# Performance work log

Hardware: AMD Instinct MI355X
Metric: run time of the kernel (lower is better)

The kernel has to match this reference:

```python
import jax, jax.numpy as jnp
import numpy as np

B, S, D = 2, 2048, 1024
N, M, HD = 16, 4, 64          # query heads, kv heads, head dim
G = N // M                    # GQA group size
V = 32000
GIN = 12                      # gate input dim
ROPE_THETA = 1024.0
ROT = int(HD * 0.5)           # partial rotary dim = 32
EPS = 1e-6
STD = 0.006


def setup_inputs() -> dict:
    key = jax.random.key(0)
    ks = jax.random.split(key, 10)
    tn = lambda k, shape: (STD * jax.random.truncated_normal(k, -3, 3, shape)).astype(jnp.float32)
    return {
        "x": jax.random.normal(ks[0], (B, S, D), jnp.float32),
        "token_ids": jax.random.randint(ks[1], (B, S), 0, V),
        "mask": jnp.tril(jnp.ones((S, S), dtype=bool)),  # causal
        "w_q": tn(ks[2], (D, N * HD)),
        "w_k": tn(ks[3], (D, M * HD)),
        "w_v": tn(ks[4], (D, M * HD)),
        "w_o": tn(ks[5], (N * HD, D)),  # zeros at init; random for a meaningful baseline
        "ve_embed": tn(ks[6], (V, M * HD)),
        "value_lambda": jnp.full((), 0.5, jnp.float32),
        "ve_lambda": jnp.full((), 0.5, jnp.float32),
        "ve_gate": tn(ks[7], (GIN, M)),
        "attn_gate": tn(ks[8], (GIN, N)),
    }


def _qk_norm(t):
    var = jnp.mean(jnp.square(t.astype(jnp.float32)), axis=-1, keepdims=True)
    return (t * jax.lax.rsqrt(var + EPS)).astype(t.dtype)


def _rope(t):
    # partial rotary: rotate first ROT dims only
    half = ROT // 2
    inv_freq = 1.0 / ROPE_THETA ** (jnp.arange(half, dtype=jnp.float32) / half)
    ang = jnp.arange(S, dtype=jnp.float32)[:, None] * inv_freq[None, :]
    cos = jnp.cos(ang)[None, :, None, :]  # [1,S,1,half]
    sin = jnp.sin(ang)[None, :, None, :]
    rot, pas = t[..., :ROT], t[..., ROT:]
    x1, x2 = jnp.split(rot, 2, axis=-1)
    return jnp.concatenate([x1 * cos - x2 * sin, x2 * cos + x1 * sin, pas], axis=-1)


def reference(x, token_ids, mask, w_q, w_k, w_v, w_o, ve_embed,
              value_lambda, ve_lambda, ve_gate, attn_gate):
    q = (x @ w_q).reshape(B, S, N, HD)
    k = (x @ w_k).reshape(B, S, M, HD)
    v = (x @ w_v).reshape(B, S, M, HD)
    q = _rope(_qk_norm(q))
    k = _rope(_qk_norm(k))

    # value-embedding lambda mixing with sigmoid gate
    ve = ve_embed[token_ids].reshape(B, S, M, HD)
    ve_g = 2.0 * jax.nn.sigmoid(x[..., :GIN] @ ve_gate)       # [B,S,M]
    v = value_lambda * v + ve_lambda * ve_g[..., None] * ve

    # GQA causal attention (group q heads over kv heads, no kv repeat)
    qg = q.reshape(B, S, M, G, HD)
    scale = 1.0 / np.sqrt(HD).astype(np.float32)
    scores = jnp.einsum('bqmgd,bkmd->bmgqk', qg, k) * scale   # [B,M,G,S,S]
    scores = jnp.where(mask[None, None, None], scores, jnp.float32(-1e30))
    p = jax.nn.softmax(scores, axis=-1)
    attn = jnp.einsum('bmgqk,bkmd->bqmgd', p, v).reshape(B, S, N, HD)

    # output sigmoid gate then out-projection
    a_g = 2.0 * jax.nn.sigmoid(x[..., :GIN] @ attn_gate)      # [B,S,N]
    attn = a_g[..., None] * attn
    return attn.reshape(B, S, N * HD) @ w_o
```

## Files before the change

### kernel.cpp

```cpp
#include <hip/hip_runtime.h>
#include <math.h>

#define S_LEN 2048
#define NHEADS 16
#define KVH 4

typedef __attribute__((ext_vector_type(8))) _Float16 half8;
typedef __attribute__((ext_vector_type(4))) _Float16 half4;
typedef __attribute__((ext_vector_type(2))) __fp16 fp16x2;
typedef __attribute__((ext_vector_type(4))) float f32x4;

__device__ inline void gld16(const void* g, void* l) {
  __builtin_amdgcn_global_load_lds(
      (const __attribute__((address_space(1))) unsigned int*)g,
      (__attribute__((address_space(3))) unsigned int*)l, 16, 0, 0);
}

__global__ __launch_bounds__(256) void setup_fused(
    const float* __restrict__ wq, const float* __restrict__ wk,
    const float* __restrict__ wv, const float* __restrict__ wo,
    const float* __restrict__ x, const float* __restrict__ attn_gate,
    _Float16* __restrict__ wqkvT, _Float16* __restrict__ woT,
    float2* __restrict__ costab, float* __restrict__ ag,
    _Float16* __restrict__ xh)
{
  const int t = threadIdx.x;
  int L = blockIdx.x;

  if (L >= 1024) {
    const size_t i = ((size_t)(L - 1024) * 256 + t) * 16;
    #pragma unroll
    for (int c = 0; c < 2; c++) {
      float4 f0 = *(const float4*)(x + i + c * 8);
      float4 f1 = *(const float4*)(x + i + c * 8 + 4);
      half8 h;
      h[0] = (_Float16)f0.x; h[1] = (_Float16)f0.y; h[2] = (_Float16)f0.z; h[3] = (_Float16)f0.w;
      h[4] = (_Float16)f1.x; h[5] = (_Float16)f1.y; h[6] = (_Float16)f1.z; h[7] = (_Float16)f1.w;
      *(half8*)(xh + i + c * 8) = h;
    }
    return;
  }
  if (L >= 768) {
    const int row = (L - 768) * 16 + (t >> 4);
    const int n = t & 15;
    float z = 0.f;
    #pragma unroll
    for (int i = 0; i < 12; ++i) z += x[(size_t)row * 1024 + i] * attn_gate[i * NHEADS + n];
    ag[(size_t)row * NHEADS + n] = 2.f / (1.f + __expf(-z));
    return;
  }
  if (L >= 640) {
    const int gi = (L - 640) * 256 + t;
    const int s = gi >> 4, i = gi & 15;
    const float ang = (float)s * exp2f(-0.625f * (float)i);
    float c, sn;
    sincosf(ang, &sn, &c);
    costab[gi] = make_float2(c, sn);
    return;
  }

  const float* in; _Float16* out; int C, ct, rt;
  if (L < 256)      { in = wq; out = wqkvT;                       C = 1024; ct = (L & 15) * 64; rt = (L >> 4) * 64; }
  else if (L < 320) { L -= 256; in = wk; out = wqkvT + (size_t)1024 * 1024; C = 256; ct = (L & 3) * 64; rt = (L >> 2) * 64; }
  else if (L < 384) { L -= 320; in = wv; out = wqkvT + (size_t)1280 * 1024; C = 256; ct = (L & 3) * 64; rt = (L >> 2) * 64; }
  else              { L -= 384; in = wo; out = woT;               C = 1024; ct = (L & 15) * 64; rt = (L >> 4) * 64; }

  __shared__ float Ls[64][65];
  {
    const int r = t >> 2, cs = (t & 3) << 4;
    const float* src = in + (size_t)(rt + r) * C + ct + cs;
    #pragma unroll
    for (int j = 0; j < 16; j += 4) {
      float4 v = *(const float4*)(src + j);
      Ls[r][cs + j] = v.x; Ls[r][cs + j + 1] = v.y;
      Ls[r][cs + j + 2] = v.z; Ls[r][cs + j + 3] = v.w;
    }
  }
  __syncthreads();
  {
    const int c = t >> 2, rs = (t & 3) << 4;
    half8 h0, h1;
    #pragma unroll
    for (int j = 0; j < 8; j++) h0[j] = (_Float16)Ls[rs + j][c];
    #pragma unroll
    for (int j = 0; j < 8; j++) h1[j] = (_Float16)Ls[rs + 8 + j][c];
    _Float16* dst = out + (size_t)(ct + c) * 1024 + rt + rs;
    *(half8*)dst = h0;
    *(half8*)(dst + 8) = h1;
  }
}

template<typename OUT_T, bool EPI>
__global__ __launch_bounds__(256) void gemm_k(
    const _Float16* __restrict__ A, const _Float16* __restrict__ BT,
    OUT_T* __restrict__ C, int M, int N, int K, int lda,
    const float2* __restrict__ costab)
{
  __shared__ _Float16 lds[16384];
  const int t = threadIdx.x;
  const int w = t >> 6, l = t & 63;
  const int lg = l >> 4, ll = l & 15;
  const int bm = blockIdx.y * 128, bn = blockIdx.x * 128;
  const int wr = (w >> 1) * 64, wc = (w & 1) * 64;
  const int srow = t >> 2, sslot = t & 3;

  f32x4 acc[4][4] = {};

  auto stage = [&](int k0, int buf) {
    char* Ab = (char*)lds + buf * 8192;
    char* Bb = (char*)lds + 16384 + buf * 8192;
    const int so = (sslot ^ (srow & 3)) << 3;
    gld16(A  + (size_t)(bm + srow)      * lda + k0 + so, Ab + w * 1024);
    gld16(A  + (size_t)(bm + srow + 64) * lda + k0 + so, Ab + 4096 + w * 1024);
    gld16(BT + (size_t)(bn + srow)      * K   + k0 + so, Bb + w * 1024);
    gld16(BT + (size_t)(bn + srow + 64) * K   + k0 + so, Bb + 4096 + w * 1024);
  };

  stage(0, 0);
  __syncthreads();

  int buf = 0;
  for (int k0 = 0; k0 < K; k0 += 32) {
    if (k0 + 32 < K) stage(k0 + 32, buf ^ 1);

    const char* Ab = (const char*)lds + buf * 8192;
    const char* Bb = (const char*)lds + 16384 + buf * 8192;
    half8 af[4], bfr[4];
    #pragma unroll
    for (int mt = 0; mt < 4; mt++) {
      const int row = wr + mt * 16 + ll;
      af[mt] = *(const half8*)(Ab + row * 64 + ((lg ^ (row & 3)) << 4));
    }
    #pragma unroll
    for (int nt = 0; nt < 4; nt++) {
      const int row = wc + nt * 16 + ll;
      bfr[nt] = *(const half8*)(Bb + row * 64 + ((lg ^ (row & 3)) << 4));
    }
    __builtin_amdgcn_s_setprio(1);
    #pragma unroll
    for (int mt = 0; mt < 4; mt++)
      #pragma unroll
      for (int nt = 0; nt < 4; nt++)
        acc[mt][nt] = __builtin_amdgcn_mfma_f32_16x16x32_f16(af[mt], bfr[nt], acc[mt][nt], 0, 0, 0);
    __builtin_amdgcn_s_setprio(0);

    __syncthreads();
    buf ^= 1;
  }

  if constexpr (EPI) {
    const int col0 = bn + wc;
    const int head = col0 >> 6;
    const bool isv = head >= 20;
    const float qs = (head < 16) ? 0.18033688f : 1.0f;
    #pragma unroll
    for (int mt = 0; mt < 4; mt++) {
      if (isv) {
        #pragma unroll
        for (int r = 0; r < 4; r++) {
          const size_t row = (size_t)bm + wr + mt * 16 + lg * 4 + r;
          #pragma unroll
          for (int nt = 0; nt < 4; nt++)
            C[row * N + col0 + nt * 16 + ll] = (OUT_T)acc[mt][nt][r];
        }
      } else {
        float ss[4];
        #pragma unroll
        for (int r = 0; r < 4; r++)
          ss[r] = acc[mt][0][r] * acc[mt][0][r] + acc[mt][1][r] * acc[mt][1][r]
                + acc[mt][2][r] * acc[mt][2][r] + acc[mt][3][r] * acc[mt][3][r];
        #pragma unroll
        for (int mi = 0; mi < 4; mi++) {
          const int msk = 1 << mi;
          #pragma unroll
          for (int r = 0; r < 4; r++) ss[r] += __shfl_xor(ss[r], msk);
        }
        #pragma unroll
        for (int r = 0; r < 4; r++) {
          const size_t row = (size_t)bm + wr + mt * 16 + lg * 4 + r;
          const float inv = rsqrtf(ss[r] * (1.0f / 64.0f) + 1e-6f) * qs;
          const float2 cs2 = costab[(row & (S_LEN - 1)) * 16 + ll];
          const float a0 = acc[mt][0][r] * inv, a1 = acc[mt][1][r] * inv;
          C[row * N + col0 +      ll] = (OUT_T)(a0 * cs2.x - a1 * cs2.y);
          C[row * N + col0 + 16 + ll] = (OUT_T)(a1 * cs2.x + a0 * cs2.y);
          C[row * N + col0 + 32 + ll] = (OUT_T)(acc[mt][2][r] * inv);
          C[row * N + col0 + 48 + ll] = (OUT_T)(acc[mt][3][r] * inv);
        }
      }
    }
  } else {
    #pragma unroll
    for (int mt = 0; mt < 4; mt++) {
      #pragma unroll
      for (int r = 0; r < 4; r++) {
        const size_t row = (size_t)bm + wr + mt * 16 + lg * 4 + r;
        #pragma unroll
        for (int nt = 0; nt < 4; nt++) {
          const int col = bn + wc + nt * 16 + ll;
          if constexpr (sizeof(OUT_T) == 2) C[row * N + col] = (OUT_T)(_Float16)acc[mt][nt][r];
          else                              C[row * N + col] = acc[mt][nt][r];
        }
      }
    }
  }
}

__global__ __launch_bounds__(256) void vtrans_mix(
    const _Float16* __restrict__ qkv, const float* __restrict__ x,
    const int* __restrict__ token_ids, const float* __restrict__ ve_embed,
    const float* __restrict__ ve_gate, const float* __restrict__ vlam,
    const float* __restrict__ velam, _Float16* __restrict__ vT)
{
  __shared__ _Float16 Ls[64][72];
  __shared__ float veg[64];
  __shared__ int toks[64];
  const int st = blockIdx.x * 64;
  const int bm = blockIdx.y;
  const int b = bm >> 2, m = bm & 3;
  const int t = threadIdx.x;

  if (t < 64) {
    const size_t row_g = (size_t)b * S_LEN + st + t;
    toks[t] = token_ids[row_g];
    float z = 0.f;
    #pragma unroll
    for (int i = 0; i < 12; ++i) z += x[row_g * 1024 + i] * ve_gate[i * KVH + m];
    veg[t] = velam[0] * 2.f / (1.f + __expf(-z));
  }
  __syncthreads();
  {
    const int sr = t >> 2, ds = (t & 3) << 4;
    const float vl = vlam[0];
    const _Float16* src = qkv + ((size_t)(b * S_LEN + st + sr)) * 1536 + 1280 + m * 64 + ds;
    const float* ves = ve_embed + (size_t)toks[sr] * 256 + m * 64 + ds;
    half8 v0 = *(const half8*)src;
    half8 v1 = *(const half8*)(src + 8);
    const float g = veg[sr];
    #pragma unroll
    for (int q4 = 0; q4 < 4; q4++) {
      float4 ev = *(const float4*)(ves + q4 * 4);
      const int o0 = q4 * 4;
      Ls[sr][ds + o0 + 0] = (_Float16)(vl * (float)((o0 + 0 < 8) ? v0[o0 + 0] : v1[o0 - 8]) + g * ev.x);
      Ls[sr][ds + o0 + 1] = (_Float16)(vl * (float)((o0 + 1 < 8) ? v0[o0 + 1] : v1[o0 - 7]) + g * ev.y);
      Ls[sr][ds + o0 + 2] = (_Float16)(vl * (float)((o0 + 2 < 8) ? v0[o0 + 2] : v1[o0 - 6]) + g * ev.z);
      Ls[sr][ds + o0 + 3] = (_Float16)(vl * (float)((o0 + 3 < 8) ? v0[o0 + 3] : v1[o0 - 5]) + g * ev.w);
    }
  }
  __syncthreads();
  {
    const int dr = t >> 2, ssl = (t & 3) << 4;
    half8 o0, o1;
    #pragma unroll
    for (int j = 0; j < 8; j++) { o0[j] = Ls[ssl + j][dr]; o1[j] = Ls[ssl + 8 + j][dr]; }
    _Float16* dst = vT + ((size_t)bm * 64 + dr) * S_LEN + st + ssl;
    *(half8*)dst = o0;
    *(half8*)(dst + 8) = o1;
  }
}

__global__ __launch_bounds__(256) void attn_mfma(
    _Float16* __restrict__ qkv, const _Float16* __restrict__ vT,
    const float* __restrict__ ag)
{
  const int L = blockIdx.x;
  const int qt = 31 - (L >> 5);
  const int b = (L >> 4) & 1;
  const int n = L & 15;
  const int m = n >> 2;

  const int t = threadIdx.x, w = t >> 6, l = t & 63;
  const int lg = l >> 4, ll = l & 15;

  __shared__ _Float16 lds[20480];

  const int qbase = qt * 64 + w * 16;
  const size_t qrow_g = (size_t)(b * S_LEN) + qbase;

  half8 qa[2];
  #pragma unroll
  for (int s = 0; s < 2; s++)
    qa[s] = *(const half8*)(qkv + (qrow_g + ll) * 1536 + n * 64 + s * 32 + lg * 8);

  float agr[4];
  #pragma unroll
  for (int r = 0; r < 4; r++)
    agr[r] = ag[(qrow_g + lg * 4 + r) * NHEADS + n];

  half8 ones;
  #pragma unroll
  for (int i = 0; i < 8; i++) ones[i] = (_Float16)1.0f;

  f32x4 o[4] = {};
  f32x4 ol = {};

  const int srow = l >> 3, sslot = l & 7;
  const int q_loc = w * 16 + ll;

  auto stage = [&](int kt, int buf) {
    #pragma unroll
    for (int i = 0; i < 2; i++) {
      const int kr = w * 16 + i * 8 + srow;
      const size_t kg = ((size_t)(b * S_LEN + kt * 64 + kr)) * 1536 + 1024 + m * 64
                        + ((sslot ^ (kr & 7)) << 3);
      gld16(qkv + kg, (char*)lds + buf * 8192 + w * 2048 + i * 1024);
      const int vr = w * 16 + i * 8 + srow;
      const size_t vg = ((size_t)((b * KVH + m) * 64 + vr)) * S_LEN + kt * 64
                        + ((sslot ^ (vr & 7)) << 3);
      gld16(vT + vg, (char*)lds + 16384 + buf * 8192 + w * 2048 + i * 1024);
    }
  };

  stage(0, 0);
  __syncthreads();

  for (int kt = 0; kt <= qt; kt++) {
    const int cur = kt & 1;
    if (kt < qt) stage(kt + 1, cur ^ 1);

    const char* Ksb = (const char*)lds + cur * 8192;
    const char* Vsb = (const char*)lds + 16384 + cur * 8192;
    char* Psb = (char*)lds + 32768;

    f32x4 sc[4];
    #pragma unroll
    for (int kf = 0; kf < 4; kf++) {
      sc[kf][0] = -11.6f; sc[kf][1] = -11.6f; sc[kf][2] = -11.6f; sc[kf][3] = -11.6f;
    }
    __builtin_amdgcn_s_setprio(1);
    #pragma unroll
    for (int s = 0; s < 2; s++)
      #pragma unroll
      for (int kf = 0; kf < 4; kf++) {
        const int krow = kf * 16 + ll;
        const half8 kb = *(const half8*)(Ksb + krow * 128
                          + (((4 * s + lg) ^ (krow & 7)) << 4));
        sc[kf] = __builtin_amdgcn_mfma_f32_16x16x32_f16(kb, qa[s], sc[kf], 0, 0, 0);
      }
    __builtin_amdgcn_s_setprio(0);

    if (kt == qt) {
      const int qg = qbase + ll;
      #pragma unroll
      for (int kf = 0; kf < 4; kf++)
        #pragma unroll
        for (int r = 0; r < 4; r++)
          if (kt * 64 + kf * 16 + 4 * lg + r > qg) sc[kf][r] = -1e30f;
    }

    #pragma unroll
    for (int kf = 0; kf < 4; kf++) {
      union { fp16x2 h2[2]; half4 h4; } P;
      P.h2[0] = __builtin_amdgcn_cvt_pkrtz(exp2f(sc[kf][0]), exp2f(sc[kf][1]));
      P.h2[1] = __builtin_amdgcn_cvt_pkrtz(exp2f(sc[kf][2]), exp2f(sc[kf][3]));
      const int slot = (2 * kf + (lg >> 1)) ^ (q_loc & 7);
      *(half4*)(Psb + q_loc * 128 + slot * 16 + (lg & 1) * 8) = P.h4;
    }

    __builtin_amdgcn_s_setprio(1);
    #pragma unroll
    for (int s = 0; s < 2; s++) {
      const half8 pa = *(const half8*)(Psb + q_loc * 128
                        + (((4 * s + lg) ^ (q_loc & 7)) << 4));
      ol = __builtin_amdgcn_mfma_f32_16x16x32_f16(pa, ones, ol, 0, 0, 0);
      #pragma unroll
      for (int df = 0; df < 4; df++) {
        const int vrow = df * 16 + ll;
        const half8 vb = *(const half8*)(Vsb + vrow * 128
                          + (((4 * s + lg) ^ (vrow & 7)) << 4));
        o[df] = __builtin_amdgcn_mfma_f32_16x16x32_f16(pa, vb, o[df], 0, 0, 0);
      }
    }
    __builtin_amdgcn_s_setprio(0);

    __syncthreads();
  }

  #pragma unroll
  for (int r = 0; r < 4; r++) {
    const size_t qrow = qrow_g + lg * 4 + r;
    const float scale = agr[r] / ol[r];
    #pragma unroll
    for (int df = 0; df < 4; df++)
      qkv[qrow * 1536 + n * 64 + df * 16 + ll] = (_Float16)(o[df][r] * scale);
  }
}

extern "C" void kernel_launch(void* const* d_in, const int* in_sizes, int n_in,
                              void* d_out, int out_size, void* d_ws, size_t ws_size,
                              hipStream_t stream) {
  const float* x         = (const float*)d_in[0];
  const int*   token_ids = (const int*)d_in[1];
  const float* w_q       = (const float*)d_in[3];
  const float* w_k       = (const float*)d_in[4];
  const float* w_v       = (const float*)d_in[5];
  const float* w_o       = (const float*)d_in[6];
  const float* ve_embed  = (const float*)d_in[7];
  const float* vlam      = (const float*)d_in[8];
  const float* velam     = (const float*)d_in[9];
  const float* ve_gate   = (const float*)d_in[10];
  const float* attn_gate = (const float*)d_in[11];
  float* out = (float*)d_out;

  char* p = (char*)d_ws;
  _Float16* wqkvT = (_Float16*)p; p += (size_t)1536 * 1024 * 2;
  _Float16* woT   = (_Float16*)p; p += (size_t)1024 * 1024 * 2;
  _Float16* qkv   = (_Float16*)p; p += (size_t)4096 * 1536 * 2;
  _Float16* vTb   = (_Float16*)p; p += (size_t)8 * 64 * S_LEN * 2;
  float*    ag    = (float*)p;    p += (size_t)4096 * NHEADS * 4;

  _Float16* xh = (_Float16*)d_out;
  float2* costab = (float2*)((char*)d_out + (size_t)12 * 1024 * 1024);

  dim3 blk(256);
  setup_fused<<<dim3(2048), blk, 0, stream>>>(w_q, w_k, w_v, w_o, x, attn_gate,
                                              wqkvT, woT, costab, ag, xh);

  gemm_k<_Float16, true><<<dim3(12, 32), blk, 0, stream>>>(
      xh, wqkvT, qkv, 4096, 1536, 1024, 1024, costab);

  vtrans_mix<<<dim3(32, 8), blk, 0, stream>>>(qkv, x, token_ids, ve_embed,
                                              ve_gate, vlam, velam, vTb);

  attn_mfma<<<dim3(1024), blk, 0, stream>>>(qkv, vTb, ag);

  gemm_k<float, false><<<dim3(8, 32), blk, 0, stream>>>(
      qkv, woT, out, 4096, 1024, 1024, 1536, nullptr);
}
```

Before: 100.0 us.

## Give each attention wave two query tiles and halve block size to 128

The attention kernel now runs 2 waves per block instead of 4, and each wave handles 32 query rows as two 16-row fragments. Each K and V fragment read from LDS is reused by two MFMAs, and staging issues four loads per thread instead of two. The aim is to cut LDS read traffic per MFMA and increase instruction-level parallelism. In exchange each wave holds more registers and there are fewer waves per block to hide latency.

```diff
diff --git a/kernel.cpp b/kernel.cpp
--- a/kernel.cpp
+++ b/kernel.cpp
@@ -258,7 +258,7 @@
   }
 }
 
-__global__ __launch_bounds__(256) void attn_mfma(
+__global__ __launch_bounds__(128) void attn_mfma(
     _Float16* __restrict__ qkv, const _Float16* __restrict__ vT,
     const float* __restrict__ ag)
 {
@@ -273,40 +273,42 @@
 
   __shared__ _Float16 lds[20480];
 
-  const int qbase = qt * 64 + w * 16;
+  const int qbase = qt * 64 + w * 32;
   const size_t qrow_g = (size_t)(b * S_LEN) + qbase;
 
-  half8 qa[2];
+  half8 qa[2][2];
   #pragma unroll
-  for (int s = 0; s < 2; s++)
-    qa[s] = *(const half8*)(qkv + (qrow_g + ll) * 1536 + n * 64 + s * 32 + lg * 8);
-
-  float agr[4];
+  for (int qf = 0; qf < 2; qf++)
+    #pragma unroll
+    for (int s = 0; s < 2; s++)
+      qa[qf][s] = *(const half8*)(qkv + (qrow_g + qf * 16 + ll) * 1536 + n * 64 + s * 32 + lg * 8);
+
+  float agr[2][4];
   #pragma unroll
-  for (int r = 0; r < 4; r++)
-    agr[r] = ag[(qrow_g + lg * 4 + r) * NHEADS + n];
+  for (int qf = 0; qf < 2; qf++)
+    #pragma unroll
+    for (int r = 0; r < 4; r++)
+      agr[qf][r] = ag[(qrow_g + qf * 16 + lg * 4 + r) * NHEADS + n];
 
   half8 ones;
   #pragma unroll
   for (int i = 0; i < 8; i++) ones[i] = (_Float16)1.0f;
 
-  f32x4 o[4] = {};
-  f32x4 ol = {};
+  f32x4 o[2][4] = {};
+  f32x4 ol[2] = {};
 
   const int srow = l >> 3, sslot = l & 7;
-  const int q_loc = w * 16 + ll;
 
   auto stage = [&](int kt, int buf) {
     #pragma unroll
-    for (int i = 0; i < 2; i++) {
-      const int kr = w * 16 + i * 8 + srow;
+    for (int i = 0; i < 4; i++) {
+      const int kr = w * 32 + i * 8 + srow;
       const size_t kg = ((size_t)(b * S_LEN + kt * 64 + kr)) * 1536 + 1024 + m * 64
                         + ((sslot ^ (kr & 7)) << 3);
-      gld16(qkv + kg, (char*)lds + buf * 8192 + w * 2048 + i * 1024);
-      const int vr = w * 16 + i * 8 + srow;
-      const size_t vg = ((size_t)((b * KVH + m) * 64 + vr)) * S_LEN + kt * 64
-                        + ((sslot ^ (vr & 7)) << 3);
-      gld16(vT + vg, (char*)lds + 16384 + buf * 8192 + w * 2048 + i * 1024);
+      gld16(qkv + kg, (char*)lds + buf * 8192 + w * 4096 + i * 1024);
+      const size_t vg = ((size_t)((b * KVH + m) * 64 + kr)) * S_LEN + kt * 64
+                        + ((sslot ^ (kr & 7)) << 3);
+      gld16(vT + vg, (char*)lds + 16384 + buf * 8192 + w * 4096 + i * 1024);
     }
   };
 
@@ -321,11 +323,14 @@
     const char* Vsb = (const char*)lds + 16384 + cur * 8192;
     char* Psb = (char*)lds + 32768;
 
-    f32x4 sc[4];
-    #pragma unroll
-    for (int kf = 0; kf < 4; kf++) {
-      sc[kf][0] = -11.6f; sc[kf][1] = -11.6f; sc[kf][2] = -11.6f; sc[kf][3] = -11.6f;
-    }
+    f32x4 sc[2][4];
+    #pragma unroll
+    for (int qf = 0; qf < 2; qf++)
+      #pragma unroll
+      for (int kf = 0; kf < 4; kf++) {
+        sc[qf][kf][0] = -11.6f; sc[qf][kf][1] = -11.6f;
+        sc[qf][kf][2] = -11.6f; sc[qf][kf][3] = -11.6f;
+      }
     __builtin_amdgcn_s_setprio(1);
     #pragma unroll
     for (int s = 0; s < 2; s++)
@@ -334,40 +339,54 @@
         const int krow = kf * 16 + ll;
         const half8 kb = *(const half8*)(Ksb + krow * 128
                           + (((4 * s + lg) ^ (krow & 7)) << 4));
-        sc[kf] = __builtin_amdgcn_mfma_f32_16x16x32_f16(kb, qa[s], sc[kf], 0, 0, 0);
+        sc[0][kf] = __builtin_amdgcn_mfma_f32_16x16x32_f16(kb, qa[0][s], sc[0][kf], 0, 0, 0);
+        sc[1][kf] = __builtin_amdgcn_mfma_f32_16x16x32_f16(kb, qa[1][s], sc[1][kf], 0, 0, 0);
       }
     __builtin_amdgcn_s_setprio(0);
 
     if (kt == qt) {
-      const int qg = qbase + ll;
-      #pragma unroll
-      for (int kf = 0; kf < 4; kf++)
-        #pragma unroll
-        for (int r = 0; r < 4; r++)
-          if (kt * 64 + kf * 16 + 4 * lg + r > qg) sc[kf][r] = -1e30f;
-    }
-
-    #pragma unroll
-    for (int kf = 0; kf < 4; kf++) {
-      union { fp16x2 h2[2]; half4 h4; } P;
-      P.h2[0] = __builtin_amdgcn_cvt_pkrtz(exp2f(sc[kf][0]), exp2f(sc[kf][1]));
-      P.h2[1] = __builtin_amdgcn_cvt_pkrtz(exp2f(sc[kf][2]), exp2f(sc[kf][3]));
-      const int slot = (2 * kf + (lg >> 1)) ^ (q_loc & 7);
-      *(half4*)(Psb + q_loc * 128 + slot * 16 + (lg & 1) * 8) = P.h4;
+      #pragma unroll
+      for (int qf = 0; qf < 2; qf++) {
+        const int qg = qbase + qf * 16 + ll;
+        #pragma unroll
+        for (int kf = 0; kf < 4; kf++)
+          #pragma unroll
+          for (int r = 0; r < 4; r++)
+            if (kt * 64 + kf * 16 + 4 * lg + r > qg) sc[qf][kf][r] = -1e30f;
+      }
+    }
+
+    #pragma unroll
+    for (int qf = 0; qf < 2; qf++) {
+      const int q_loc = w * 32 + qf * 16 + ll;
+      #pragma unroll
+      for (int kf = 0; kf < 4; kf++) {
+        union { fp16x2 h2[2]; half4 h4; } P;
+        P.h2[0] = __builtin_amdgcn_cvt_pkrtz(exp2f(sc[qf][kf][0]), exp2f(sc[qf][kf][1]));
+        P.h2[1] = __builtin_amdgcn_cvt_pkrtz(exp2f(sc[qf][kf][2]), exp2f(sc[qf][kf][3]));
+        const int slot = (2 * kf + (lg >> 1)) ^ (q_loc & 7);
+        *(half4*)(Psb + q_loc * 128 + slot * 16 + (lg & 1) * 8) = P.h4;
+      }
     }
 
     __builtin_amdgcn_s_setprio(1);
     #pragma unroll
     for (int s = 0; s < 2; s++) {
-      const half8 pa = *(const half8*)(Psb + q_loc * 128
-                        + (((4 * s + lg) ^ (q_loc & 7)) << 4));
-      ol = __builtin_amdgcn_mfma_f32_16x16x32_f16(pa, ones, ol, 0, 0, 0);
+      half8 pa[2];
+      #pragma unroll
+      for (int qf = 0; qf < 2; qf++) {
+        const int prow = w * 32 + qf * 16 + ll;
+        pa[qf] = *(const half8*)(Psb + prow * 128 + (((4 * s + lg) ^ (prow & 7)) << 4));
+      }
+      ol[0] = __builtin_amdgcn_mfma_f32_16x16x32_f16(pa[0], ones, ol[0], 0, 0, 0);
+      ol[1] = __builtin_amdgcn_mfma_f32_16x16x32_f16(pa[1], ones, ol[1], 0, 0, 0);
       #pragma unroll
       for (int df = 0; df < 4; df++) {
         const int vrow = df * 16 + ll;
         const half8 vb = *(const half8*)(Vsb + vrow * 128
                           + (((4 * s + lg) ^ (vrow & 7)) << 4));
-        o[df] = __builtin_amdgcn_mfma_f32_16x16x32_f16(pa, vb, o[df], 0, 0, 0);
+        o[0][df] = __builtin_amdgcn_mfma_f32_16x16x32_f16(pa[0], vb, o[0][df], 0, 0, 0);
+        o[1][df] = __builtin_amdgcn_mfma_f32_16x16x32_f16(pa[1], vb, o[1][df], 0, 0, 0);
       }
     }
     __builtin_amdgcn_s_setprio(0);
@@ -376,13 +395,15 @@
   }
 
   #pragma unroll
-  for (int r = 0; r < 4; r++) {
-    const size_t qrow = qrow_g + lg * 4 + r;
-    const float scale = agr[r] / ol[r];
-    #pragma unroll
-    for (int df = 0; df < 4; df++)
-      qkv[qrow * 1536 + n * 64 + df * 16 + ll] = (_Float16)(o[df][r] * scale);
-  }
+  for (int qf = 0; qf < 2; qf++)
+    #pragma unroll
+    for (int r = 0; r < 4; r++) {
+      const size_t qrow = qrow_g + qf * 16 + lg * 4 + r;
+      const float scale = agr[qf][r] / ol[qf][r];
+      #pragma unroll
+      for (int df = 0; df < 4; df++)
+        qkv[qrow * 1536 + n * 64 + df * 16 + ll] = (_Float16)(o[qf][df][r] * scale);
+    }
 }
 
 extern "C" void kernel_launch(void* const* d_in, const int* in_sizes, int n_in,
@@ -421,7 +442,7 @@
   vtrans_mix<<<dim3(32, 8), blk, 0, stream>>>(qkv, x, token_ids, ve_embed,
                                               ve_gate, vlam, velam, vTb);
 
-  attn_mfma<<<dim3(1024), blk, 0, stream>>>(qkv, vTb, ag);
+  attn_mfma<<<dim3(1024), dim3(128), 0, stream>>>(qkv, vTb, ag);
 
   gemm_k<float, false><<<dim3(8, 32), blk, 0, stream>>>(
       qkv, woT, out, 4096, 1024, 1024, 1536, nullptr);
```

Measured after the change: 111.2 us. 11.1% more time.
